# Optimization experiments

Measured on AMD Instinct MI355X. Metric: run time of the kernel, lower is better.

The kernel has to match this reference:

```python
import jax, jax.numpy as jnp
import numpy as np

B, N, K = 4, 4096, 16
DP, DM = 128, 256  # d_points, d_model


def setup_inputs() -> dict:
    key = jax.random.key(0)
    ks = jax.random.split(key, 10)
    w = lambda k, s: (jax.random.normal(k, s) * 0.02).astype(jnp.float32)
    return dict(
        features=jax.random.normal(ks[0], (B, N, DP), dtype=jnp.float32),
        xyz=jax.random.normal(ks[1], (B, N, 3), dtype=jnp.float32),
        fc1_w=w(ks[2], (DP, DM)), fc1_b=jnp.zeros((DM,), jnp.float32),
        fc2_w=w(ks[3], (DM, DP)), fc2_b=jnp.zeros((DP,), jnp.float32),
        fd1_w=w(ks[4], (3, DM)), fd1_b=jnp.zeros((DM,), jnp.float32),
        fd2_w=w(ks[5], (DM, DM)), fd2_b=jnp.zeros((DM,), jnp.float32),
        wq=w(ks[6], (DM, DM)), wk=w(ks[7], (DM, DM)), wv=w(ks[8], (DM, DM)),
    )


def reference(features, xyz, fc1_w, fc1_b, fc2_w, fc2_b,
              fd1_w, fd1_b, fd2_w, fd2_b, wq, wk, wv):
    # KNN of xyz against itself (includes self, distance-sorted ascending)
    sq = jnp.sum(xyz * xyz, axis=-1)                                 # [B,N]
    d2 = sq[:, :, None] + sq[:, None, :] - 2.0 * jnp.einsum('bnc,bmc->bnm', xyz, xyz)
    _, knn_idx = jax.lax.top_k(-d2, K)                               # [B,N,K]
    gather = jax.vmap(lambda pts, idx: pts[idx])                     # [B,N,C],[B,N,K]->[B,N,K,C]
    knn_xyz = gather(xyz, knn_idx)                                   # [B,N,K,3]

    x = features @ fc1_w + fc1_b                                     # [B,N,DM]
    q = x @ wq                                                       # [B,N,DM]
    kf = gather(x @ wk, knn_idx)                                     # [B,N,K,DM]
    vf = gather(x @ wv, knn_idx)                                     # [B,N,K,DM]

    delta = xyz[:, :, None, :] - knn_xyz                             # [B,N,K,3]
    pos = jax.nn.relu(delta @ fd1_w + fd1_b) @ fd2_w + fd2_b         # [B,N,K,DM]

    logits = jnp.einsum('bnd,bnkd->bnk', q, kf + pos) / np.sqrt(DM).astype(np.float32)
    attn = jax.nn.softmax(logits, axis=-1)                           # [B,N,K]
    res = jnp.einsum('bnk,bnkd->bnd', attn, vf + pos)                # [B,N,DM]

    out = res @ fc2_w + fc2_b + features                             # [B,N,DP]
    return jnp.transpose(out, (0, 2, 1))                             # [B,DP,N]
```

## Files before the change

### kernel.cpp

```cpp
#include <hip/hip_runtime.h>
#include <hip/hip_bf16.h>
#include <hip/hip_fp16.h>
#include <math.h>

#define B_   4
#define N_   4096
#define K_   16
#define DP_  128
#define DM_  256
#define NPTS (B_ * N_)
#define SEG_ 16
#define CAND_ (N_ / SEG_)
#define QPAD 136

typedef unsigned int u32;
typedef unsigned char u8;
typedef _Float16 f16;
typedef __attribute__((ext_vector_type(2))) __fp16 h2;
typedef __attribute__((ext_vector_type(8))) _Float16 f16x8;
typedef __attribute__((ext_vector_type(4))) float floatx4;

static __device__ __forceinline__ h2 pkrtz(float a, float b) {
    return __builtin_amdgcn_cvt_pkrtz(a, b);
}
static __device__ __forceinline__ u32 asu32(h2 h) { return __builtin_bit_cast(u32, h); }
static __device__ __forceinline__ h2 ash2(u32 u) { return __builtin_bit_cast(h2, u); }

#define CEXA(x, y) { u32 _lo = min(x, y); y = max(x, y); x = _lo; }
#define CEXD(x, y) { u32 _hi = max(x, y); y = min(x, y); x = _hi; }

static __device__ __forceinline__ void sort16_desc(u32 c[16]) {
    CEXD(c[0],c[1]);  CEXD(c[2],c[3]);  CEXD(c[4],c[5]);  CEXD(c[6],c[7]);
    CEXD(c[8],c[9]);  CEXD(c[10],c[11]); CEXD(c[12],c[13]); CEXD(c[14],c[15]);
    CEXD(c[0],c[2]);  CEXD(c[1],c[3]);  CEXD(c[4],c[6]);  CEXD(c[5],c[7]);
    CEXD(c[8],c[10]); CEXD(c[9],c[11]); CEXD(c[12],c[14]); CEXD(c[13],c[15]);
    CEXD(c[1],c[2]);  CEXD(c[5],c[6]);  CEXD(c[9],c[10]); CEXD(c[13],c[14]);
    CEXD(c[0],c[4]);  CEXD(c[1],c[5]);  CEXD(c[2],c[6]);  CEXD(c[3],c[7]);
    CEXD(c[8],c[12]); CEXD(c[9],c[13]); CEXD(c[10],c[14]); CEXD(c[11],c[15]);
    CEXD(c[2],c[4]);  CEXD(c[3],c[5]);  CEXD(c[10],c[12]); CEXD(c[11],c[13]);
    CEXD(c[1],c[2]);  CEXD(c[3],c[4]);  CEXD(c[5],c[6]);
    CEXD(c[9],c[10]); CEXD(c[11],c[12]); CEXD(c[13],c[14]);
    CEXD(c[0],c[8]);  CEXD(c[1],c[9]);  CEXD(c[2],c[10]); CEXD(c[3],c[11]);
    CEXD(c[4],c[12]); CEXD(c[5],c[13]); CEXD(c[6],c[14]); CEXD(c[7],c[15]);
    CEXD(c[4],c[8]);  CEXD(c[5],c[9]);  CEXD(c[6],c[10]); CEXD(c[7],c[11]);
    CEXD(c[2],c[4]);  CEXD(c[3],c[5]);  CEXD(c[6],c[8]);  CEXD(c[7],c[9]);
    CEXD(c[10],c[12]); CEXD(c[11],c[13]);
    CEXD(c[1],c[2]);  CEXD(c[3],c[4]);  CEXD(c[5],c[6]);  CEXD(c[7],c[8]);
    CEXD(c[9],c[10]); CEXD(c[11],c[12]); CEXD(c[13],c[14]);
}

static __device__ __forceinline__ void remerge16_asc(u32 L[16]) {
    CEXA(L[0],L[8]);  CEXA(L[1],L[9]);  CEXA(L[2],L[10]); CEXA(L[3],L[11]);
    CEXA(L[4],L[12]); CEXA(L[5],L[13]); CEXA(L[6],L[14]); CEXA(L[7],L[15]);
    CEXA(L[0],L[4]);  CEXA(L[1],L[5]);  CEXA(L[2],L[6]);  CEXA(L[3],L[7]);
    CEXA(L[8],L[12]); CEXA(L[9],L[13]); CEXA(L[10],L[14]); CEXA(L[11],L[15]);
    CEXA(L[0],L[2]);  CEXA(L[1],L[3]);  CEXA(L[4],L[6]);  CEXA(L[5],L[7]);
    CEXA(L[8],L[10]); CEXA(L[9],L[11]); CEXA(L[12],L[14]); CEXA(L[13],L[15]);
    CEXA(L[0],L[1]);  CEXA(L[2],L[3]);  CEXA(L[4],L[5]);  CEXA(L[6],L[7]);
    CEXA(L[8],L[9]);  CEXA(L[10],L[11]); CEXA(L[12],L[13]); CEXA(L[14],L[15]);
}

static __device__ void knn_part_body(float4* sc, const float* __restrict__ xyz,
                                     u32* __restrict__ part, int id)
{
    const int xblk = id & 15;
    const int s = (id >> 4) & 15;
    const int b = id >> 8;
    const int n = xblk * 256 + threadIdx.x;
    const float* xb = xyz + (size_t)b * N_ * 3;
    const float x0 = xb[n * 3 + 0], x1 = xb[n * 3 + 1], x2 = xb[n * 3 + 2];
    const float nx0 = -x0, nx1 = -x1, nx2 = -x2;
    const float hs = 0.5f * fmaf(x0, x0, fmaf(x1, x1, x2 * x2));
    const u32 kmask = 0xFFFFF000u;

    {
        const int m = s * CAND_ + threadIdx.x;
        const float a0 = xb[m * 3 + 0];
        const float a1 = xb[m * 3 + 1];
        const float a2 = xb[m * 3 + 2];
        sc[threadIdx.x] = make_float4(a0, a1, a2, 0.5f * (a0 * a0 + a1 * a1 + a2 * a2));
    }
    __syncthreads();

    u32 L[16];
#pragma unroll
    for (int i = 0; i < 16; ++i) L[i] = 0xFFFFFFFFu;

    const u32 ibase = (u32)(s * CAND_);
    for (int m0 = 0; m0 < CAND_; m0 += 16) {
        float4 cc[16];
#pragma unroll
        for (int t = 0; t < 16; ++t) cc[t] = sc[m0 + t];
        u32 c[16];
#pragma unroll
        for (int t = 0; t < 16; ++t) {
            const float e = fmaf(nx0, cc[t].x,
                            fmaf(nx1, cc[t].y,
                            fmaf(nx2, cc[t].z, cc[t].w + hs)));
            c[t] = (__float_as_uint(fmaxf(e, 0.0f)) & kmask) | (ibase + (u32)(m0 + t));
        }
        sort16_desc(c);
#pragma unroll
        for (int i = 0; i < 16; ++i) L[i] = min(L[i], c[i]);
        remerge16_asc(L);
    }

    const int p = b * N_ + n;
#pragma unroll
    for (int j = 0; j < 16; ++j)
        part[(size_t)(s * 16 + j) * NPTS + p] = L[j];
}

static __device__ void prep_body(float (*t)[33],
    const float* __restrict__ wq, const float* __restrict__ wk, const float* __restrict__ wv,
    const float* __restrict__ fd2, const float* __restrict__ fc1, const float* __restrict__ fc2,
    const float* __restrict__ feat,
    f16* __restrict__ catW, f16* __restrict__ fc2T, f16* __restrict__ bt2,
    f16* __restrict__ fd2c, f16* __restrict__ wqc, f16* __restrict__ fc1c,
    f16* __restrict__ featb, int bx, int by, int job)
{
    const int tid = threadIdx.x;

    if (job < 4) {
        const float* in; int R, C;
        switch (job) {
            case 0: in = wq;  R = DM_; C = DM_; break;
            case 1: in = wk;  R = DM_; C = DM_; break;
            case 2: in = wv;  R = DM_; C = DM_; break;
            default: in = fc2; R = DM_; C = DP_; break;
        }
        const int c0 = bx * 32, r0 = by * 32;
        if (c0 >= C || r0 >= R) return;
        const int lx = tid & 31, ly = tid >> 5;
#pragma unroll
        for (int i = 0; i < 32; i += 8)
            t[ly + i][lx] = in[(size_t)(r0 + ly + i) * C + c0 + lx];
        __syncthreads();
#pragma unroll
        for (int i = 0; i < 32; i += 8) {
            const int c = c0 + ly + i;
            const f16 v = (f16)t[lx][ly + i];
            int n;
            switch (job) {
                case 0: n = c; break;
                case 1: n = 256 + ((c >> 2) << 3) + (c & 3); break;
                case 2: n = 256 + ((c >> 2) << 3) + 4 + (c & 3); break;
                default: n = -1; break;
            }
            if (job < 3) {
                catW[(size_t)n * DM_ + r0 + lx] = v;
            } else {
                fc2T[(size_t)c * DM_ + r0 + lx] = v;
                bt2[(size_t)c * 512 + 256 + r0 + lx] = v;
            }
        }
    } else {
        const int bid = by * 8 + bx;
        const int tId = bid * 256 + tid;
        const float* in; f16* outp; int n4;
        if (job == 4)      { in = fd2;  outp = fd2c;  n4 = (DM_ * DM_) / 4; }
        else if (job == 5) { in = wq;   outp = wqc;   n4 = (DM_ * DM_) / 4; }
        else if (job == 6) { in = fc1;  outp = fc1c;  n4 = (DP_ * DM_) / 4; }
        else               { in = feat; outp = featb; n4 = (NPTS * DP_) / 4; }
        for (int i = tId; i < n4; i += 16384) {
            const float4 v = ((const float4*)in)[i];
            const u32 lo = asu32(pkrtz(v.x, v.y));
            const u32 hi = asu32(pkrtz(v.z, v.w));
            ((uint2*)outp)[i] = make_uint2(lo, hi);
        }
    }
}

__global__ __launch_bounds__(256) void fused_prep_knn_kernel(
    const float* __restrict__ wq, const float* __restrict__ wk, const float* __restrict__ wv,
    const float* __restrict__ fd2, const float* __restrict__ fc1, const float* __restrict__ fc2,
    const float* __restrict__ feat,
    f16* __restrict__ catW, f16* __restrict__ fc2T, f16* __restrict__ bt2,
    f16* __restrict__ fd2c, f16* __restrict__ wqc, f16* __restrict__ fc1c,
    f16* __restrict__ featb,
    const float* __restrict__ xyz, u32* __restrict__ part)
{
    __shared__ __align__(16) char smem[4352];
    const int id = blockIdx.x;
    if (id < 512) {
        prep_body((float(*)[33])smem, wq, wk, wv, fd2, fc1, fc2, feat,
                  catW, fc2T, bt2, fd2c, wqc, fc1c, featb,
                  id & 7, (id >> 3) & 7, id >> 6);
    } else {
        knn_part_body((float4*)smem, xyz, part, id - 512);
    }
}

static __device__ void gemm_tile(f16* As, f16* Bs,
    const f16* __restrict__ A, const f16* __restrict__ Bt,
    f16* __restrict__ Cb,
    int M, int N, int K, int ldc, int bx, int by)
{
    const int tid = threadIdx.x;
    const int m0 = by * 128, n0 = bx * 128;
    const int w = tid >> 6, l = tid & 63;
    const int wm = (w >> 1) * 64, wn = (w & 1) * 64;
    const int fm = l & 15, kq = l >> 4;

    floatx4 acc[4][4];
#pragma unroll
    for (int i = 0; i < 4; ++i)
#pragma unroll
        for (int j = 0; j < 4; ++j)
            acc[i][j] = (floatx4){0.0f, 0.0f, 0.0f, 0.0f};

    for (int k0 = 0; k0 < K; k0 += 32) {
        __syncthreads();
#pragma unroll
        for (int c = 0; c < 2; ++c) {
            const int li = tid + c * 256;
            const int row = li >> 2, part = li & 3;
            *(uint4*)&As[row * 32 + part * 8] =
                *(const uint4*)&A[(size_t)(m0 + row) * K + k0 + part * 8];
            *(uint4*)&Bs[row * 32 + part * 8] =
                *(const uint4*)&Bt[(size_t)(n0 + row) * K + k0 + part * 8];
        }
        __syncthreads();
        f16x8 af[4], bf[4];
#pragma unroll
        for (int i = 0; i < 4; ++i)
            af[i] = *(const f16x8*)&As[(wm + i * 16 + fm) * 32 + kq * 8];
#pragma unroll
        for (int j = 0; j < 4; ++j)
            bf[j] = *(const f16x8*)&Bs[(wn + j * 16 + fm) * 32 + kq * 8];
#pragma unroll
        for (int i = 0; i < 4; ++i)
#pragma unroll
            for (int j = 0; j < 4; ++j)
                acc[i][j] = __builtin_amdgcn_mfma_f32_16x16x32_f16(af[i], bf[j], acc[i][j], 0, 0, 0);
    }

#pragma unroll
    for (int i = 0; i < 4; ++i) {
#pragma unroll
        for (int j = 0; j < 4; ++j) {
            const int col = n0 + wn + j * 16 + fm;
            const int rowb = m0 + wm + i * 16 + kq * 4;
#pragma unroll
            for (int r = 0; r < 4; ++r)
                Cb[(size_t)(rowb + r) * ldc + col] = (f16)acc[i][j][r];
        }
    }
}

static __device__ void mergeAB_body(const u32* __restrict__ part, int* __restrict__ knn_idx,
                                    int id)
{
    const int p = id * 256 + threadIdx.x;
    const int b = p >> 12;

    u32 L[16];
#pragma unroll
    for (int i = 0; i < 16; ++i) L[i] = 0xFFFFFFFFu;

    for (int s = 0; s < SEG_; ++s) {
        u32 seg[16];
#pragma unroll
        for (int j = 0; j < 16; ++j)
            seg[j] = part[(size_t)(s * 16 + j) * NPTS + p];
#pragma unroll
        for (int i = 0; i < 16; ++i) L[i] = min(L[i], seg[15 - i]);
        remerge16_asc(L);
    }

    int* o = knn_idx + (size_t)p * K_;
#pragma unroll
    for (int i = 0; i < 16; ++i) o[i] = b * N_ + (int)(L[i] & 0xFFFu);
}

#define KVP 520
__global__ __launch_bounds__(256) void gemm_qkv_fused_kernel(
    const f16* __restrict__ A,
    const f16* __restrict__ Bt,
    const float* __restrict__ bias,
    const float* __restrict__ xyz,
    const float* __restrict__ fd1_w, const float* __restrict__ fd1_b,
    f16* __restrict__ Cb,
    u8* __restrict__ kvw, f16* __restrict__ ubuf,
    const u32* __restrict__ part, int* __restrict__ knn_idx)
{
    __shared__ __align__(16) f16 As[64 * 136];
    __shared__ __align__(16) f16 Bs[128 * 136];
    __shared__ __align__(16) f16 kvs[64 * KVP];
    const int bid = blockIdx.x;
    if (bid >= 256) { mergeAB_body(part, knn_idx, bid - 256); return; }

    const int tid = threadIdx.x;
    const int m0 = bid * 64;
    const int w = tid >> 6, l = tid & 63;
    const int wr = (w >> 1) * 32;
    const int wn = (w & 1) * 64;
    const int fm = l & 15, kq = l >> 4;

#pragma unroll
    for (int c = 0; c < 4; ++c) {
        const int li = tid + c * 256;
        const int row = li >> 4, pt = li & 15;
        *(uint4*)&As[row * 136 + pt * 8] =
            *(const uint4*)&A[(size_t)(m0 + row) * 128 + pt * 8];
    }

    for (int nt = 0; nt < 8; ++nt) {
        __syncthreads();
#pragma unroll
        for (int c = 0; c < 8; ++c) {
            const int li = tid + c * 256;
            const int row = li >> 4, pt = li & 15;
            *(uint4*)&Bs[row * 136 + pt * 8] =
                *(const uint4*)&Bt[(size_t)(nt * 128 + row) * 128 + pt * 8];
        }
        __syncthreads();

        floatx4 acc[2][4];
#pragma unroll
        for (int i = 0; i < 2; ++i)
#pragma unroll
            for (int j = 0; j < 4; ++j)
                acc[i][j] = (floatx4){0.0f, 0.0f, 0.0f, 0.0f};

#pragma unroll
        for (int kk = 0; kk < 4; ++kk) {
            f16x8 af[2], bf[4];
#pragma unroll
            for (int i = 0; i < 2; ++i)
                af[i] = *(const f16x8*)&As[(wr + i * 16 + fm) * 136 + kk * 32 + kq * 8];
#pragma unroll
            for (int j = 0; j < 4; ++j)
                bf[j] = *(const f16x8*)&Bs[(wn + j * 16 + fm) * 136 + kk * 32 + kq * 8];
#pragma unroll
            for (int i = 0; i < 2; ++i)
#pragma unroll
                for (int j = 0; j < 4; ++j)
                    acc[i][j] = __builtin_amdgcn_mfma_f32_16x16x32_f16(af[i], bf[j], acc[i][j], 0, 0, 0);
        }

        if (nt >= 2 && nt < 6) {
#pragma unroll
            for (int i = 0; i < 2; ++i) {
#pragma unroll
                for (int j = 0; j < 4; ++j) {
                    const int col = nt * 128 + wn + j * 16 + fm;
                    const int lcol = col - 256;
                    const int rowb = wr + i * 16 + kq * 4;
#pragma unroll
                    for (int r = 0; r < 4; ++r)
                        kvs[(rowb + r) * KVP + lcol] = (f16)(acc[i][j][r] + bias[col]);
                }
            }
        } else {
#pragma unroll
            for (int i = 0; i < 2; ++i) {
#pragma unroll
                for (int j = 0; j < 4; ++j) {
                    const int col = nt * 128 + wn + j * 16 + fm;
                    const int rowb = m0 + wr + i * 16 + kq * 4;
#pragma unroll
                    for (int r = 0; r < 4; ++r)
                        Cb[(size_t)(rowb + r) * 1024 + col] = (f16)(acc[i][j][r] + bias[col]);
                }
            }
        }
    }
    __syncthreads();

    for (int it = 0; it < 16; ++it) {
        const int task = it * 256 + tid;
        const int pl = task >> 6, g = task & 63;
        const int p = m0 + pl;
        const uint4 kv = *(const uint4*)&kvs[pl * KVP + g * 8];
        const h2 k01 = ash2(kv.x), k23 = ash2(kv.y), v01 = ash2(kv.z), v23 = ash2(kv.w);
        int lo = 0, hi = 0;
        lo = __builtin_amdgcn_cvt_pk_fp8_f32((float)k01.x, (float)k01.y, lo, false);
        lo = __builtin_amdgcn_cvt_pk_fp8_f32((float)k23.x, (float)k23.y, lo, true);
        hi = __builtin_amdgcn_cvt_pk_fp8_f32((float)v01.x, (float)v01.y, hi, false);
        hi = __builtin_amdgcn_cvt_pk_fp8_f32((float)v23.x, (float)v23.y, hi, true);

        const float x0 = xyz[(size_t)p * 3 + 0];
        const float x1 = xyz[(size_t)p * 3 + 1];
        const float x2 = xyz[(size_t)p * 3 + 2];
        const int c0 = g * 4;
        const float4 w0v = *(const float4*)&fd1_w[c0];
        const float4 w1v = *(const float4*)&fd1_w[DM_ + c0];
        const float4 w2v = *(const float4*)&fd1_w[2 * DM_ + c0];
        const float4 b1v = *(const float4*)&fd1_b[c0];
        const float ww0 = x0 * w0v.x + x1 * w1v.x + x2 * w2v.x;
        const float ww1 = x0 * w0v.y + x1 * w1v.y + x2 * w2v.y;
        const float ww2 = x0 * w0v.z + x1 * w1v.z + x2 * w2v.z;
        const float ww3 = x0 * w0v.w + x1 * w1v.w + x2 * w2v.w;

        uint4 row;
        row.x = (u32)lo;
        row.y = (u32)hi;
        row.z = asu32(pkrtz(ww0, ww1));
        row.w = asu32(pkrtz(ww2, ww3));
        *(uint4*)(kvw + (size_t)p * 1024 + g * 16) = row;

        const uint2 uu = make_uint2(asu32(pkrtz(ww0 + b1v.x, ww1 + b1v.y)),
                                    asu32(pkrtz(ww2 + b1v.z, ww3 + b1v.w)));
        *(uint2*)(ubuf + (size_t)p * 256 + c0) = uu;
    }
}

__global__ __launch_bounds__(256) void gemm_out_kernel(
    const f16* __restrict__ A,
    const f16* __restrict__ Bt,
    const float* __restrict__ bias2,
    const float* __restrict__ feat,
    float* __restrict__ CT)
{
    __shared__ __align__(16) f16 As[64 * 32];
    __shared__ __align__(16) f16 Bs[128 * 32];
    const int tid = threadIdx.x;
    const int m0 = blockIdx.x * 64;
    const int w = tid >> 6, l = tid & 63;
    const int wn = w * 32;
    const int fm = l & 15, kq = l >> 4;

    floatx4 acc[4][2];
#pragma unroll
    for (int i = 0; i < 4; ++i)
#pragma unroll
        for (int j = 0; j < 2; ++j)
            acc[i][j] = (floatx4){0.0f, 0.0f, 0.0f, 0.0f};

    for (int k0 = 0; k0 < 512; k0 += 32) {
        __syncthreads();
        {
            const int row = tid >> 2, part = tid & 3;
            *(uint4*)&As[row * 32 + part * 8] =
                *(const uint4*)&A[(size_t)(m0 + row) * 512 + k0 + part * 8];
        }
#pragma unroll
        for (int c = 0; c < 2; ++c) {
            const int li = tid + c * 256;
            const int row = li >> 2, part = li & 3;
            *(uint4*)&Bs[row * 32 + part * 8] =
                *(const uint4*)&Bt[(size_t)row * 512 + k0 + part * 8];
        }
        __syncthreads();
        f16x8 af[4], bf[2];
#pragma unroll
        for (int i = 0; i < 4; ++i)
            af[i] = *(const f16x8*)&As[(i * 16 + fm) * 32 + kq * 8];
#pragma unroll
        for (int j = 0; j < 2; ++j)
            bf[j] = *(const f16x8*)&Bs[(wn + j * 16 + fm) * 32 + kq * 8];
#pragma unroll
        for (int i = 0; i < 4; ++i)
#pragma unroll
            for (int j = 0; j < 2; ++j)
                acc[i][j] = __builtin_amdgcn_mfma_f32_16x16x32_f16(af[i], bf[j], acc[i][j], 0, 0, 0);
    }

#pragma unroll
    for (int i = 0; i < 4; ++i) {
#pragma unroll
        for (int j = 0; j < 2; ++j) {
            const int col = wn + j * 16 + fm;
            const int rowb = m0 + i * 16 + kq * 4;
            float4 vv;
#pragma unroll
            for (int r = 0; r < 4; ++r)
                ((float*)&vv)[r] = acc[i][j][r] + bias2[col]
                                 + feat[(size_t)(rowb + r) * DP_ + col];
            const int bb = rowb >> 12;
            *(float4*)&CT[(size_t)(bb * DP_ + col) * N_ + (rowb & (N_ - 1))] = vv;
        }
    }
}

__global__ __launch_bounds__(256) void fused_small1_kernel(
    const f16* __restrict__ fd2c, const f16* __restrict__ wqc,
    f16* __restrict__ catWqp,
    const f16* __restrict__ fc2T, f16* __restrict__ bt2)
{
    __shared__ __align__(16) f16 As[128 * 32];
    __shared__ __align__(16) f16 Bs[128 * 32];
    const int id = blockIdx.x;
    if (id < 4)
        gemm_tile(As, Bs, fd2c, wqc, catWqp, DM_, DM_, DM_, DM_, id & 1, id >> 1);
    else
        gemm_tile(As, Bs, fc2T, fd2c, bt2, DP_, DM_, DM_, 512, id - 4, 0);
}

__global__ __launch_bounds__(256) void fused_small2_kernel(
    const f16* __restrict__ catW, const f16* __restrict__ fc1c, f16* __restrict__ WallT,
    const float* __restrict__ fc1_b, const float* __restrict__ fd2_b,
    const float* __restrict__ fc2_w, const float* __restrict__ fc2_b,
    float* __restrict__ b_all, float* __restrict__ bias2)
{
    __shared__ __align__(16) f16 As[128 * 32];
    __shared__ __align__(16) f16 Bs[128 * 32];
    const int id = blockIdx.x;
    const int tid = threadIdx.x;
    if (id < 8) {
        gemm_tile(As, Bs, catW, fc1c, WallT, 1024, DP_, DM_, DP_, 0, id);
    } else if (id < 12) {
        const int n = (id - 8) * 256 + tid;
        float s = 0.0f;
        for (int j = 0; j < DM_; ++j)
            s += fc1_b[j] * (float)catW[(size_t)n * DM_ + j];
        b_all[n] = s;
    } else if (tid < DP_) {
        float s = fc2_b[tid];
        for (int t = 0; t < DM_; ++t)
            s += fd2_b[t] * fc2_w[(size_t)t * DP_ + tid];
        bias2[tid] = s;
    }
}

__global__ __launch_bounds__(256, 1) void attn_kernel(
    const f16* __restrict__ qkv, const u8* __restrict__ kvw,
    const f16* __restrict__ ubuf, const int* __restrict__ knn_idx,
    const float* __restrict__ fd2_b,
    f16* __restrict__ ab)
{
    const int wave = threadIdx.x >> 6, l = threadIdx.x & 63;
    const int bi = blockIdx.x;
    const int p = ((bi & 3) << 12) + ((bi >> 2) << 2) + wave;
    const int c0 = l * 4;

    int gi = 0;
    if (l < 16) gi = knn_idx[p * K_ + l];

    uint4 kvr[16];
#pragma unroll
    for (int k = 0; k < 16; ++k) {
        const int gik = __shfl(gi, k);
        kvr[k] = *(const uint4*)(kvw + (size_t)gik * 1024 + l * 16);
    }
    asm volatile("" ::: "memory");

    const uint2 qu  = *(const uint2*)(qkv + (size_t)p * 1024 + c0);
    const uint2 qpu = *(const uint2*)(qkv + (size_t)p * 1024 + 768 + c0);
    const uint2 uu  = *(const uint2*)(ubuf + (size_t)p * 256 + c0);
    const h2 qh01 = ash2(qu.x), qh23 = ash2(qu.y);
    const h2 qp01 = ash2(qpu.x), qp23 = ash2(qpu.y);
    const h2 u01 = ash2(uu.x), u23 = ash2(uu.y);
    const float q0 = (float)qh01.x, q1 = (float)qh01.y, q2 = (float)qh23.x, q3 = (float)qh23.y;
    const h2 zero2 = (h2)(__fp16)0.0f;

    const float4 f2b = *(const float4*)&fd2_b[c0];

    float qb;
    {
        float tq = q0 * f2b.x + q1 * f2b.y + q2 * f2b.z + q3 * f2b.w;
#pragma unroll
        for (int off = 1; off < 64; off <<= 1) tq += __shfl_xor(tq, off);
        qb = tq;
    }

    float lg[16];
    u32 h01r[16], h23r[16];
#pragma unroll
    for (int k = 0; k < 16; ++k) {
        const uint4 r = kvr[k];
        h2 d01 = u01 - ash2(r.z);
        h2 d23 = u23 - ash2(r.w);
        d01 = __builtin_elementwise_max(d01, zero2);
        d23 = __builtin_elementwise_max(d23, zero2);
        h01r[k] = asu32(d01); h23r[k] = asu32(d23);
        const auto k01 = __builtin_amdgcn_cvt_pk_f32_fp8((int)r.x, false);
        const auto k23 = __builtin_amdgcn_cvt_pk_f32_fp8((int)r.x, true);
        float t = q0 * k01[0] + q1 * k01[1] + q2 * k23[0] + q3 * k23[1];
        t = __builtin_amdgcn_fdot2(d01, qp01, t, false);
        t = __builtin_amdgcn_fdot2(d23, qp23, t, false);
#pragma unroll
        for (int off = 1; off < 64; off <<= 1) t += __shfl_xor(t, off);
        lg[k] = t;
    }

    float att[16];
    {
        float mx = -3.0e38f;
#pragma unroll
        for (int k = 0; k < 16; ++k) {
            att[k] = (lg[k] + qb) * (1.0f / 16.0f);
            mx = fmaxf(mx, att[k]);
        }
        float s = 0.0f;
#pragma unroll
        for (int k = 0; k < 16; ++k) { att[k] = __expf(att[k] - mx); s += att[k]; }
        const float inv = 1.0f / s;
#pragma unroll
        for (int k = 0; k < 16; ++k) att[k] *= inv;
    }

    float rb[4] = {0, 0, 0, 0}, hb[4] = {0, 0, 0, 0};
#pragma unroll
    for (int k = 0; k < 16; ++k) {
        const auto v01 = __builtin_amdgcn_cvt_pk_f32_fp8((int)kvr[k].y, false);
        const auto v23 = __builtin_amdgcn_cvt_pk_f32_fp8((int)kvr[k].y, true);
        const h2 hh01 = ash2(h01r[k]), hh23 = ash2(h23r[k]);
        const float a = att[k];
        rb[0] = fmaf(a, v01[0], rb[0]);
        rb[1] = fmaf(a, v01[1], rb[1]);
        rb[2] = fmaf(a, v23[0], rb[2]);
        rb[3] = fmaf(a, v23[1], rb[3]);
        hb[0] = fmaf(a, (float)hh01.x, hb[0]);
        hb[1] = fmaf(a, (float)hh01.y, hb[1]);
        hb[2] = fmaf(a, (float)hh23.x, hb[2]);
        hb[3] = fmaf(a, (float)hh23.y, hb[3]);
    }

    const uint2 ho = make_uint2(asu32(pkrtz(hb[0], hb[1])), asu32(pkrtz(hb[2], hb[3])));
    const uint2 ro = make_uint2(asu32(pkrtz(rb[0], rb[1])), asu32(pkrtz(rb[2], rb[3])));
    *(uint2*)(ab + (size_t)p * 512 + c0) = ho;
    *(uint2*)(ab + (size_t)p * 512 + 256 + c0) = ro;
}

extern "C" void kernel_launch(void* const* d_in, const int* in_sizes, int n_in,
                              void* d_out, int out_size, void* d_ws, size_t ws_size,
                              hipStream_t stream)
{
    const float* features = (const float*)d_in[0];
    const float* xyz   = (const float*)d_in[1];
    const float* fc1_w = (const float*)d_in[2];
    const float* fc1_b = (const float*)d_in[3];
    const float* fc2_w = (const float*)d_in[4];
    const float* fc2_b = (const float*)d_in[5];
    const float* fd1_w = (const float*)d_in[6];
    const float* fd1_b = (const float*)d_in[7];
    const float* fd2_w = (const float*)d_in[8];
    const float* fd2_b = (const float*)d_in[9];
    const float* wq    = (const float*)d_in[10];
    const float* wk    = (const float*)d_in[11];
    const float* wv    = (const float*)d_in[12];
    float* out = (float*)d_out;

    char* base = (char*)d_ws;
    const size_t MB = 1024 * 1024;
    u32*  part = (u32*)(base + 0);
    f16*  ab   = (f16*)(base + 0);
    u8*   kvw  = (u8*)(base + 20 * MB);
    f16*  qkv  = (f16*)(base + 36 * MB);
    f16*  featb = (f16*)(base + 68 * MB);
    int*  idx  = (int*)(base + 72 * MB);
    char* wb = base + 73 * MB;
    f16* catW  = (f16*)(wb + 0);
    f16* WallT = (f16*)(wb + 512 * 1024);
    f16* bt2   = (f16*)(wb + 768 * 1024);
    f16* fd2c  = (f16*)(wb + 896 * 1024);
    f16* wqc   = (f16*)(wb + 1024 * 1024);
    f16* fc1c  = (f16*)(wb + 1152 * 1024);
    f16* fc2T  = (f16*)(wb + 1216 * 1024);
    float* b_all = (float*)(wb + 1280 * 1024);
    float* bias2 = (float*)(wb + 1284 * 1024);
    f16*  ubuf = (f16*)(base + 76 * MB);

    const dim3 blk(256);

    fused_prep_knn_kernel<<<dim3(512 + 1024), blk, 0, stream>>>(
        wq, wk, wv, fd2_w, fc1_w, fc2_w, features,
        catW, fc2T, bt2, fd2c, wqc, fc1c, featb, xyz, part);
    fused_small1_kernel<<<dim3(6), blk, 0, stream>>>(fd2c, wqc, catW + 768 * 256, fc2T, bt2);
    fused_small2_kernel<<<dim3(13), blk, 0, stream>>>(catW, fc1c, WallT,
                                                      fc1_b, fd2_b, fc2_w, fc2_b, b_all, bias2);
    gemm_qkv_fused_kernel<<<dim3(256 + 64), blk, 0, stream>>>(
        featb, WallT, b_all, xyz, fd1_w, fd1_b, qkv, kvw, ubuf, part, idx);
    attn_kernel<<<dim3(NPTS / 4), blk, 0, stream>>>(qkv, kvw, ubuf, idx, fd2_b, ab);
    gemm_out_kernel<<<dim3(NPTS / 64), blk, 0, stream>>>(ab, bt2, bias2, features, out);

    (void)in_sizes; (void)n_in; (void)out_size; (void)ws_size;
}
```

Measured before the change: 213.5 us.

## Halve QKV GEMM row tile and stream K/V packing per column tile

The fused QKV GEMM kernel now uses 32-row tiles instead of 64, doubling the GEMM block count to 512. The large 64x520 K/V shared staging buffer is replaced by a small per-column-tile stage, and the fp8 packing plus position-encoding work runs right after each K/V column tile instead of in one pass at the end. This cuts shared memory per block, which should raise occupancy and spread work over more CUs. In exchange, each staged fd2 weight tile is reused across fewer rows, Bt is loaded twice as often overall, and there are extra barriers inside the column loop.

Result: faster. 203.3 us (-4.8%).

```diff
diff --git a/kernel.cpp b/kernel.cpp
--- a/kernel.cpp
+++ b/kernel.cpp
@@ -273,7 +273,6 @@
     for (int i = 0; i < 16; ++i) o[i] = b * N_ + (int)(L[i] & 0xFFFu);
 }
 
-#define KVP 520
 __global__ __launch_bounds__(256) void gemm_qkv_fused_kernel(
     const f16* __restrict__ A,
     const f16* __restrict__ Bt,
@@ -284,21 +283,21 @@
     u8* __restrict__ kvw, f16* __restrict__ ubuf,
     const u32* __restrict__ part, int* __restrict__ knn_idx)
 {
-    __shared__ __align__(16) f16 As[64 * 136];
+    __shared__ __align__(16) f16 As[32 * 136];
     __shared__ __align__(16) f16 Bs[128 * 136];
-    __shared__ __align__(16) f16 kvs[64 * KVP];
+    __shared__ __align__(16) f16 kvstage[32 * 136];
     const int bid = blockIdx.x;
-    if (bid >= 256) { mergeAB_body(part, knn_idx, bid - 256); return; }
+    if (bid >= 512) { mergeAB_body(part, knn_idx, bid - 512); return; }
 
     const int tid = threadIdx.x;
-    const int m0 = bid * 64;
+    const int m0 = bid * 32;
     const int w = tid >> 6, l = tid & 63;
-    const int wr = (w >> 1) * 32;
+    const int wr = (w >> 1) * 16;
     const int wn = (w & 1) * 64;
     const int fm = l & 15, kq = l >> 4;
 
 #pragma unroll
-    for (int c = 0; c < 4; ++c) {
+    for (int c = 0; c < 2; ++c) {
         const int li = tid + c * 256;
         const int row = li >> 4, pt = li & 15;
         *(uint4*)&As[row * 136 + pt * 8] =
@@ -316,93 +315,84 @@
         }
         __syncthreads();
 
-        floatx4 acc[2][4];
-#pragma unroll
-        for (int i = 0; i < 2; ++i)
-#pragma unroll
-            for (int j = 0; j < 4; ++j)
-                acc[i][j] = (floatx4){0.0f, 0.0f, 0.0f, 0.0f};
+        floatx4 acc[4];
+#pragma unroll
+        for (int j = 0; j < 4; ++j)
+            acc[j] = (floatx4){0.0f, 0.0f, 0.0f, 0.0f};
 
 #pragma unroll
         for (int kk = 0; kk < 4; ++kk) {
-            f16x8 af[2], bf[4];
-#pragma unroll
-            for (int i = 0; i < 2; ++i)
-                af[i] = *(const f16x8*)&As[(wr + i * 16 + fm) * 136 + kk * 32 + kq * 8];
+            f16x8 af, bf[4];
+            af = *(const f16x8*)&As[(wr + fm) * 136 + kk * 32 + kq * 8];
 #pragma unroll
             for (int j = 0; j < 4; ++j)
                 bf[j] = *(const f16x8*)&Bs[(wn + j * 16 + fm) * 136 + kk * 32 + kq * 8];
 #pragma unroll
-            for (int i = 0; i < 2; ++i)
-#pragma unroll
-                for (int j = 0; j < 4; ++j)
-                    acc[i][j] = __builtin_amdgcn_mfma_f32_16x16x32_f16(af[i], bf[j], acc[i][j], 0, 0, 0);
+            for (int j = 0; j < 4; ++j)
+                acc[j] = __builtin_amdgcn_mfma_f32_16x16x32_f16(af, bf[j], acc[j], 0, 0, 0);
         }
 
         if (nt >= 2 && nt < 6) {
 #pragma unroll
-            for (int i = 0; i < 2; ++i) {
-#pragma unroll
-                for (int j = 0; j < 4; ++j) {
-                    const int col = nt * 128 + wn + j * 16 + fm;
-                    const int lcol = col - 256;
-                    const int rowb = wr + i * 16 + kq * 4;
-#pragma unroll
-                    for (int r = 0; r < 4; ++r)
-                        kvs[(rowb + r) * KVP + lcol] = (f16)(acc[i][j][r] + bias[col]);
-                }
+            for (int j = 0; j < 4; ++j) {
+                const int col = nt * 128 + wn + j * 16 + fm;
+                const int lcol = col - nt * 128;
+                const int rowb = wr + kq * 4;
+#pragma unroll
+                for (int r = 0; r < 4; ++r)
+                    kvstage[(rowb + r) * 136 + lcol] = (f16)(acc[j][r] + bias[col]);
+            }
+            __syncthreads();
+
+#pragma unroll
+            for (int it = 0; it < 2; ++it) {
+                const int task = it * 256 + tid;
+                const int pl = task >> 4, gl = task & 15;
+                const int p = m0 + pl;
+                const int g = (nt - 2) * 16 + gl;
+                const uint4 kv = *(const uint4*)&kvstage[pl * 136 + gl * 8];
+                const h2 k01 = ash2(kv.x), k23 = ash2(kv.y);
+                const h2 v01 = ash2(kv.z), v23 = ash2(kv.w);
+                int lo = 0, hi = 0;
+                lo = __builtin_amdgcn_cvt_pk_fp8_f32((float)k01.x, (float)k01.y, lo, false);
+                lo = __builtin_amdgcn_cvt_pk_fp8_f32((float)k23.x, (float)k23.y, lo, true);
+                hi = __builtin_amdgcn_cvt_pk_fp8_f32((float)v01.x, (float)v01.y, hi, false);
+                hi = __builtin_amdgcn_cvt_pk_fp8_f32((float)v23.x, (float)v23.y, hi, true);
+
+                const float x0 = xyz[(size_t)p * 3 + 0];
+                const float x1 = xyz[(size_t)p * 3 + 1];
+                const float x2 = xyz[(size_t)p * 3 + 2];
+                const int c0 = g * 4;
+                const float4 w0v = *(const float4*)&fd1_w[c0];
+                const float4 w1v = *(const float4*)&fd1_w[DM_ + c0];
+                const float4 w2v = *(const float4*)&fd1_w[2 * DM_ + c0];
+                const float4 b1v = *(const float4*)&fd1_b[c0];
+                const float ww0 = x0 * w0v.x + x1 * w1v.x + x2 * w2v.x;
+                const float ww1 = x0 * w0v.y + x1 * w1v.y + x2 * w2v.y;
+                const float ww2 = x0 * w0v.z + x1 * w1v.z + x2 * w2v.z;
+                const float ww3 = x0 * w0v.w + x1 * w1v.w + x2 * w2v.w;
+
+                uint4 row;
+                row.x = (u32)lo;
+                row.y = (u32)hi;
+                row.z = asu32(pkrtz(ww0, ww1));
+                row.w = asu32(pkrtz(ww2, ww3));
+                *(uint4*)(kvw + (size_t)p * 1024 + g * 16) = row;
+
+                const uint2 uu = make_uint2(asu32(pkrtz(ww0 + b1v.x, ww1 + b1v.y)),
+                                            asu32(pkrtz(ww2 + b1v.z, ww3 + b1v.w)));
+                *(uint2*)(ubuf + (size_t)p * 256 + c0) = uu;
             }
         } else {
 #pragma unroll
-            for (int i = 0; i < 2; ++i) {
-#pragma unroll
-                for (int j = 0; j < 4; ++j) {
-                    const int col = nt * 128 + wn + j * 16 + fm;
-                    const int rowb = m0 + wr + i * 16 + kq * 4;
-#pragma unroll
-                    for (int r = 0; r < 4; ++r)
-                        Cb[(size_t)(rowb + r) * 1024 + col] = (f16)(acc[i][j][r] + bias[col]);
-                }
+            for (int j = 0; j < 4; ++j) {
+                const int col = nt * 128 + wn + j * 16 + fm;
+                const int rowb = m0 + wr + kq * 4;
+#pragma unroll
+                for (int r = 0; r < 4; ++r)
+                    Cb[(size_t)(rowb + r) * 1024 + col] = (f16)(acc[j][r] + bias[col]);
             }
         }
-    }
-    __syncthreads();
-
-    for (int it = 0; it < 16; ++it) {
-        const int task = it * 256 + tid;
-        const int pl = task >> 6, g = task & 63;
-        const int p = m0 + pl;
-        const uint4 kv = *(const uint4*)&kvs[pl * KVP + g * 8];
-        const h2 k01 = ash2(kv.x), k23 = ash2(kv.y), v01 = ash2(kv.z), v23 = ash2(kv.w);
-        int lo = 0, hi = 0;
-        lo = __builtin_amdgcn_cvt_pk_fp8_f32((float)k01.x, (float)k01.y, lo, false);
-        lo = __builtin_amdgcn_cvt_pk_fp8_f32((float)k23.x, (float)k23.y, lo, true);
-        hi = __builtin_amdgcn_cvt_pk_fp8_f32((float)v01.x, (float)v01.y, hi, false);
-        hi = __builtin_amdgcn_cvt_pk_fp8_f32((float)v23.x, (float)v23.y, hi, true);
-
-        const float x0 = xyz[(size_t)p * 3 + 0];
-        const float x1 = xyz[(size_t)p * 3 + 1];
-        const float x2 = xyz[(size_t)p * 3 + 2];
-        const int c0 = g * 4;
-        const float4 w0v = *(const float4*)&fd1_w[c0];
-        const float4 w1v = *(const float4*)&fd1_w[DM_ + c0];
-        const float4 w2v = *(const float4*)&fd1_w[2 * DM_ + c0];
-        const float4 b1v = *(const float4*)&fd1_b[c0];
-        const float ww0 = x0 * w0v.x + x1 * w1v.x + x2 * w2v.x;
-        const float ww1 = x0 * w0v.y + x1 * w1v.y + x2 * w2v.y;
-        const float ww2 = x0 * w0v.z + x1 * w1v.z + x2 * w2v.z;
-        const float ww3 = x0 * w0v.w + x1 * w1v.w + x2 * w2v.w;
-
-        uint4 row;
-        row.x = (u32)lo;
-        row.y = (u32)hi;
-        row.z = asu32(pkrtz(ww0, ww1));
-        row.w = asu32(pkrtz(ww2, ww3));
-        *(uint4*)(kvw + (size_t)p * 1024 + g * 16) = row;
-
-        const uint2 uu = make_uint2(asu32(pkrtz(ww0 + b1v.x, ww1 + b1v.y)),
-                                    asu32(pkrtz(ww2 + b1v.z, ww3 + b1v.w)));
-        *(uint2*)(ubuf + (size_t)p * 256 + c0) = uu;
     }
 }
 
@@ -661,7 +651,7 @@
     fused_small1_kernel<<<dim3(6), blk, 0, stream>>>(fd2c, wqc, catW + 768 * 256, fc2T, bt2);
     fused_small2_kernel<<<dim3(13), blk, 0, stream>>>(catW, fc1c, WallT,
                                                       fc1_b, fd2_b, fc2_w, fc2_b, b_all, bias2);
-    gemm_qkv_fused_kernel<<<dim3(256 + 64), blk, 0, stream>>>(
+    gemm_qkv_fused_kernel<<<dim3(512 + 64), blk, 0, stream>>>(
         featb, WallT, b_all, xyz, fd1_w, fd1_b, qkv, kvw, ubuf, part, idx);
     attn_kernel<<<dim3(NPTS / 4), blk, 0, stream>>>(qkv, kvw, ubuf, idx, fd2_b, ab);
     gemm_out_kernel<<<dim3(NPTS / 64), blk, 0, stream>>>(ab, bt2, bias2, features, out);
```
